# Kernel tuning notes

Measured on AMD Instinct MI355X. Metric: run time of the kernel, lower is better.

## Reference

```python
import jax, jax.numpy as jnp
import numpy as np

# Static discretization grid (torch version computes this on host from data;
# with inputs in [0,1) the clamps min(..,-2)-0.1 / max(..,2)+0.1 make it constant).
PPU = 128          # points_per_unit
MULT = 16          # 2 ** rho.num_halving_layers
XMIN, XMAX = -2.1, 2.1
NUM_GRID = int(np.ceil(PPU * (XMAX - XMIN) / MULT) * MULT)  # 544
SIGMA_CH = 1024
RHO_C = 8          # rho in/out channels


def setup_inputs() -> dict:
    key = jax.random.key(0)
    ks = jax.random.split(key, 8)
    B, N, M = 8, 2048, 2048
    log_ls = float(np.log(2.0 / PPU))  # init_length_scale = 2 / points_per_unit
    return {
        "x": jax.random.uniform(ks[0], (B, N, 1), dtype=jnp.float32),
        "y": jax.random.normal(ks[1], (B, N, 1), dtype=jnp.float32),
        "x_out": jax.random.uniform(ks[2], (B, M, 1), dtype=jnp.float32),
        # encoder ConvDeepSet (in_channels = 2: density + y)
        "enc_sigma": jnp.full((2,), log_ls, dtype=jnp.float32),
        "enc_W": jax.random.normal(ks[3], (2, RHO_C), dtype=jnp.float32) * 0.5,
        "enc_b": jnp.zeros((RHO_C,), dtype=jnp.float32),
        # rho stand-in: point-wise linear 8 -> 8
        "rho_W": jax.random.normal(ks[4], (RHO_C, RHO_C), dtype=jnp.float32) * 0.35,
        "rho_b": jnp.zeros((RHO_C,), dtype=jnp.float32),
        # mean FinalLayer (in_channels = rho.out_channels = 8, out_channels = 1)
        "mean_sigma": jnp.full((RHO_C,), log_ls, dtype=jnp.float32),
        "mean_W": jax.random.normal(ks[5], (RHO_C, 1), dtype=jnp.float32) * 0.35,
        "mean_b": jnp.zeros((1,), dtype=jnp.float32),
        # sigma FinalLayer (out_channels = sigma_channels = 1024)
        "sig_sigma": jnp.full((RHO_C,), log_ls, dtype=jnp.float32),
        "sig_W": jax.random.normal(ks[6], (RHO_C, SIGMA_CH), dtype=jnp.float32) * 0.35,
        "sig_b": jnp.zeros((SIGMA_CH,), dtype=jnp.float32),
        "noise_scale": jnp.zeros((1,), dtype=jnp.float32),
    }


def _rbf_weights(a, t, log_sigma):
    # a: (B, n, 1), t: (B, m, 1) -> (B, n, m, C) per-channel RBF weights
    d = (a - jnp.swapaxes(t, 1, 2)) ** 2            # (B, n, m) squared dists
    scales = jnp.exp(log_sigma)                      # (C,)
    return jnp.exp(-0.5 * d[..., None] / scales ** 2)


def reference(x, y, x_out, enc_sigma, enc_W, enc_b, rho_W, rho_b,
              mean_sigma, mean_W, mean_b, sig_sigma, sig_W, sig_b, noise_scale):
    B = x.shape[0]
    grid = jnp.broadcast_to(
        jnp.linspace(XMIN, XMAX, NUM_GRID, dtype=x.dtype)[None, :, None],
        (B, NUM_GRID, 1))

    # --- encoder ConvDeepSet: density channel + value channel, RBF smoothing onto grid
    wt = _rbf_weights(x, grid, enc_sigma)            # (B, N, G, 2)
    y_aug = jnp.concatenate([jnp.ones_like(x), y], axis=-1)  # (B, N, 2)
    F = jnp.einsum('bnc,bngc->bgc', y_aug, wt)       # (B, G, 2)
    den, conv = F[..., :1], F[..., 1:]
    F = jnp.concatenate([den, conv / (den + 1e-8)], axis=-1)
    h = jax.nn.sigmoid(F @ enc_W + enc_b)            # (B, G, 8)

    # --- rho (stand-in point-wise linear CNN)
    h = h @ rho_W + rho_b                            # (B, G, 8)

    # --- mean FinalLayer: RBF set-conv from grid to x_out, then linear
    wt_m = _rbf_weights(grid, x_out, mean_sigma)     # (B, G, M, 8)
    mean = jnp.einsum('bgc,bgmc->bmc', h, wt_m) @ mean_W + mean_b  # (B, M, 1)

    # --- sigma FinalLayer -> basis embedding, inner-product covariance
    wt_s = _rbf_weights(grid, x_out, sig_sigma)      # (B, G, M, 8)
    basis = jnp.einsum('bgc,bgmc->bmc', h, wt_s) @ sig_W + sig_b   # (B, M, 1024)
    cov = jnp.einsum('bmc,bnc->bmn', basis, basis)   # (B, M, M)
    cov = cov + jnp.exp(noise_scale[0]) * jnp.eye(cov.shape[-1], dtype=cov.dtype)
    return mean, cov
```

## Files before the change

### kernel.cpp

```cpp
#include <hip/hip_runtime.h>
#include <math.h>

#define GRID_N 544
#define BATCH  8
#define NPTS   2048
#define MPTS   2048
#define XMIN_F (-2.1f)
#define STEP_F (4.2f / 543.0f)

typedef float v4f __attribute__((ext_vector_type(4)));

#define PRM_OFF 0
#define H_OFF   128
#define FST_OFF (H_OFF + BATCH*GRID_N*8)
#define P_OFF   (FST_OFF + BATCH*8*MPTS)
#define CM_OFF  (P_OFF + BATCH*MPTS*8)

__global__ __launch_bounds__(256) void k_encode(
    const float* __restrict__ x, const float* __restrict__ y,
    const float* __restrict__ enc_sigma,
    const float* __restrict__ enc_W, const float* __restrict__ enc_b,
    const float* __restrict__ rho_W, const float* __restrict__ rho_b,
    const float* __restrict__ mean_sigma, const float* __restrict__ sig_sigma,
    const float* __restrict__ sig_W, const float* __restrict__ sig_b,
    float* __restrict__ prm, float* __restrict__ h_out) {
  int b = blockIdx.y, g = blockIdx.x, t = threadIdx.x;

  if (g == GRID_N) {
    if (b != 0) return;
    __shared__ float part[256];
    {
      int pair = t >> 2, q = t & 3;
      int i = pair >> 3, j = pair & 7;
      float s = 0.f;
      int k0 = q * 256;
      for (int k = k0; k < k0 + 256; ++k) s += sig_W[i*1024+k] * sig_W[j*1024+k];
      part[t] = s;
      __syncthreads();
      if (q == 0) prm[16 + pair] = part[t] + part[t+1] + part[t+2] + part[t+3];
      __syncthreads();
    }
    {
      int ch = t >> 5, lane = t & 31;
      float s = 0.f;
      for (int k = lane; k < 1024; k += 32) s += sig_W[ch*1024+k] * sig_b[k];
      part[t] = s;
      __syncthreads();
      if (lane == 0) {
        float acc = 0.f;
        for (int k = 0; k < 32; ++k) acc += part[(ch<<5)+k];
        prm[80 + ch] = acc;
      }
      __syncthreads();
    }
    if (t < 32) {
      float v = 0.f;
      for (int k = t; k < 1024; k += 32) v += sig_b[k] * sig_b[k];
      part[t] = v;
    }
    __syncthreads();
    if (t == 0) {
      float v = 0.f;
      for (int k = 0; k < 32; ++k) v += part[k];
      prm[88] = v;
    } else if (t == 1) {
      bool f = true;
      for (int c = 0; c < 8; ++c) {
        prm[c]     = 0.5f * __expf(-2.f * mean_sigma[c]);
        prm[8 + c] = 0.5f * __expf(-2.f * sig_sigma[c]);
        if (mean_sigma[c] != mean_sigma[0] || sig_sigma[c] != sig_sigma[0]) f = false;
      }
      if (mean_sigma[0] != sig_sigma[0]) f = false;
      prm[89] = f ? 1.f : 0.f;
    }
    return;
  }

  float gv = XMIN_F + (float)g * STEP_F;
  float es0 = enc_sigma[0], es1 = enc_sigma[1];
  float a0 = 0.5f * __expf(-2.f * es0);
  float a1 = 0.5f * __expf(-2.f * es1);
  bool uni = (es0 == es1);
  const float4* x4 = (const float4*)(x + (size_t)b * NPTS);
  const float4* y4 = (const float4*)(y + (size_t)b * NPTS);
  float s0 = 0.f, s1 = 0.f;
  #pragma unroll
  for (int i = 0; i < 2; ++i) {
    int n = i * 256 + t;
    float4 xv = x4[n], yv = y4[n];
    float dx, d, w;
    dx = xv.x - gv; d = dx*dx; w = __expf(-d*a0); s0 += w;
    s1 += yv.x * (uni ? w : __expf(-d*a1));
    dx = xv.y - gv; d = dx*dx; w = __expf(-d*a0); s0 += w;
    s1 += yv.y * (uni ? w : __expf(-d*a1));
    dx = xv.z - gv; d = dx*dx; w = __expf(-d*a0); s0 += w;
    s1 += yv.z * (uni ? w : __expf(-d*a1));
    dx = xv.w - gv; d = dx*dx; w = __expf(-d*a0); s0 += w;
    s1 += yv.w * (uni ? w : __expf(-d*a1));
  }
  #pragma unroll
  for (int off = 32; off > 0; off >>= 1) {
    s0 += __shfl_down(s0, off);
    s1 += __shfl_down(s1, off);
  }
  __shared__ float w0s[4], w1s[4];
  int wid = t >> 6;
  if ((t & 63) == 0) { w0s[wid] = s0; w1s[wid] = s1; }
  __syncthreads();
  if (t == 0) {
    float den = w0s[0] + w0s[1] + w0s[2] + w0s[3];
    float conv = w1s[0] + w1s[1] + w1s[2] + w1s[3];
    float F0 = den, F1 = conv / (den + 1e-8f);
    float hh[8];
    #pragma unroll
    for (int jj = 0; jj < 8; ++jj) {
      float z = F0 * enc_W[jj] + F1 * enc_W[8 + jj] + enc_b[jj];
      hh[jj] = 1.f / (1.f + __expf(-z));
    }
    #pragma unroll
    for (int jj = 0; jj < 8; ++jj) {
      float v = rho_b[jj];
      #pragma unroll
      for (int ii = 0; ii < 8; ++ii) v += hh[ii] * rho_W[ii*8 + jj];
      h_out[((size_t)b * GRID_N + g) * 8 + jj] = v;
    }
  }
}

__global__ __launch_bounds__(256) void k_feat(
    const float* __restrict__ x_out, const float* __restrict__ mean_W,
    const float* __restrict__ mean_b, const float* __restrict__ prm,
    const float* __restrict__ h, float* __restrict__ mean_out,
    float* __restrict__ fSt, float* __restrict__ Pv, float* __restrict__ cm) {
  int b = blockIdx.y, t = threadIdx.x;
  int ml = t & 63, slice = t >> 6;
  int m = blockIdx.x * 64 + ml;
  float xo = x_out[(size_t)b * MPTS + m];
  bool fused = prm[89] != 0.f;
  float accm[8] = {0,0,0,0,0,0,0,0};
  float accs[8] = {0,0,0,0,0,0,0,0};
  const float* hb = h + (size_t)b * GRID_N * 8;
  const float4* h4 = (const float4*)hb;
  int gbase = slice * 136;
  if (fused) {
    float a = prm[0];
    for (int gg = 0; gg < 136; ++gg) {
      int g = gbase + gg;
      float gv = XMIN_F + (float)g * STEP_F;
      float dx = gv - xo;
      float w = __expf(-(dx*dx) * a);
      float4 h0 = h4[g*2], h1 = h4[g*2+1];
      accm[0] += h0.x * w; accm[1] += h0.y * w;
      accm[2] += h0.z * w; accm[3] += h0.w * w;
      accm[4] += h1.x * w; accm[5] += h1.y * w;
      accm[6] += h1.z * w; accm[7] += h1.w * w;
    }
  } else {
    float am[8], asg[8];
    #pragma unroll
    for (int c = 0; c < 8; ++c) { am[c] = prm[c]; asg[c] = prm[8 + c]; }
    for (int gg = 0; gg < 136; ++gg) {
      int g = gbase + gg;
      float gv = XMIN_F + (float)g * STEP_F;
      float dx = gv - xo;
      float d = dx * dx;
      #pragma unroll
      for (int c = 0; c < 8; ++c) {
        float hv = hb[g*8 + c];
        accm[c] += hv * __expf(-d * am[c]);
        accs[c] += hv * __expf(-d * asg[c]);
      }
    }
  }
  __shared__ float red[256 * 17];
  #pragma unroll
  for (int c = 0; c < 8; ++c) {
    red[t*17 + c] = accm[c];
    if (!fused) red[t*17 + 8 + c] = accs[c];
  }
  __syncthreads();
  if (t < 64) {
    int mm = blockIdx.x * 64 + t;
    float fm[8], fs[8];
    #pragma unroll
    for (int c = 0; c < 8; ++c) {
      fm[c] = red[t*17+c] + red[(t+64)*17+c] + red[(t+128)*17+c] + red[(t+192)*17+c];
    }
    if (fused) {
      #pragma unroll
      for (int c = 0; c < 8; ++c) fs[c] = fm[c];
    } else {
      #pragma unroll
      for (int c = 0; c < 8; ++c) {
        fs[c] = red[t*17+8+c] + red[(t+64)*17+8+c] + red[(t+128)*17+8+c] + red[(t+192)*17+8+c];
      }
    }
    float mv = mean_b[0];
    #pragma unroll
    for (int c = 0; c < 8; ++c) mv += fm[c] * mean_W[c];
    mean_out[(size_t)b * MPTS + mm] = mv;
    float cmv = prm[88];
    #pragma unroll
    for (int c = 0; c < 8; ++c) cmv += fs[c] * prm[80 + c];
    cm[(size_t)b * MPTS + mm] = cmv;
    size_t base = ((size_t)b * MPTS + mm) * 8;
    #pragma unroll
    for (int c2 = 0; c2 < 8; ++c2) {
      float p = prm[80 + c2];
      #pragma unroll
      for (int c = 0; c < 8; ++c) p += fs[c] * prm[16 + c*8 + c2];
      Pv[base + c2] = p;
    }
    float* fp = fSt + (size_t)b * 8 * MPTS + mm;
    #pragma unroll
    for (int c = 0; c < 8; ++c) fp[c * MPTS] = fs[c];
  }
}

__global__ __launch_bounds__(256) void k_cov(
    const float* __restrict__ fSt, const float* __restrict__ Pv,
    const float* __restrict__ cm, const float* __restrict__ noise_scale,
    float* __restrict__ cov) {
  int b = blockIdx.y, t = threadIdx.x;
  int half = blockIdx.x & 1, rt = blockIdx.x >> 1;
  int col = half * 1024 + 4 * t;
  int row0 = rt * 32;
  float noise = __expf(noise_scale[0]);
  v4f fn[8];
  const float* fb = fSt + (size_t)b * 8 * MPTS;
  #pragma unroll
  for (int c = 0; c < 8; ++c)
    fn[c] = *(const v4f*)(fb + c * MPTS + col);
  const float* Pr = Pv + ((size_t)b * MPTS + row0) * 8;
  const float* Cr = cm + (size_t)b * MPTS + row0;
  #pragma unroll 1
  for (int r8 = 0; r8 < 4; ++r8) {
    v4f o[8];
    #pragma unroll
    for (int i = 0; i < 8; ++i) {
      int mi = r8 * 8 + i;
      float cc = Cr[mi];
      float a0 = cc, a1 = cc, a2 = cc, a3 = cc;
      #pragma unroll
      for (int c = 0; c < 8; ++c) {
        float p = Pr[mi * 8 + c];
        a0 += p * fn[c].x; a1 += p * fn[c].y;
        a2 += p * fn[c].z; a3 += p * fn[c].w;
      }
      int mg = row0 + mi;
      if (mg == col)     a0 += noise;
      if (mg == col + 1) a1 += noise;
      if (mg == col + 2) a2 += noise;
      if (mg == col + 3) a3 += noise;
      o[i].x = a0; o[i].y = a1; o[i].z = a2; o[i].w = a3;
    }
    #pragma unroll
    for (int i = 0; i < 8; ++i) {
      int mi = r8 * 8 + i;
      v4f* dst = (v4f*)(cov + ((size_t)b * MPTS + row0 + mi) * MPTS + col);
      __builtin_nontemporal_store(o[i], dst);
    }
  }
}

extern "C" void kernel_launch(void* const* d_in, const int* in_sizes, int n_in,
                              void* d_out, int out_size, void* d_ws, size_t ws_size,
                              hipStream_t stream) {
  const float* x          = (const float*)d_in[0];
  const float* y          = (const float*)d_in[1];
  const float* x_out      = (const float*)d_in[2];
  const float* enc_sigma  = (const float*)d_in[3];
  const float* enc_W      = (const float*)d_in[4];
  const float* enc_b      = (const float*)d_in[5];
  const float* rho_W      = (const float*)d_in[6];
  const float* rho_b      = (const float*)d_in[7];
  const float* mean_sigma = (const float*)d_in[8];
  const float* mean_W     = (const float*)d_in[9];
  const float* mean_b     = (const float*)d_in[10];
  const float* sig_sigma  = (const float*)d_in[11];
  const float* sig_W      = (const float*)d_in[12];
  const float* sig_b      = (const float*)d_in[13];
  const float* noise_sc   = (const float*)d_in[14];

  float* wsf = (float*)d_ws;
  float* prm  = wsf + PRM_OFF;
  float* hbuf = wsf + H_OFF;
  float* fStb = wsf + FST_OFF;
  float* Pb   = wsf + P_OFF;
  float* cmb  = wsf + CM_OFF;

  float* mean_out = (float*)d_out;
  float* cov_out  = mean_out + (size_t)BATCH * MPTS;

  k_encode<<<dim3(GRID_N + 1, BATCH), 256, 0, stream>>>(
      x, y, enc_sigma, enc_W, enc_b, rho_W, rho_b,
      mean_sigma, sig_sigma, sig_W, sig_b, prm, hbuf);
  k_feat<<<dim3(MPTS/64, BATCH), 256, 0, stream>>>(x_out, mean_W, mean_b, prm,
                                                   hbuf, mean_out, fStb, Pb, cmb);
  k_cov<<<dim3(2 * (MPTS/32), BATCH), 256, 0, stream>>>(fStb, Pb, cmb, noise_sc,
                                                        cov_out);
}
```

Measured before the change: 219.7 us.

## Fuse encode, feature and covariance kernels into one cooperative persistent kernel

Replaces the three separate kernel launches with a single cooperative kernel that loops persistently over the encode, feature and covariance work and separates the stages with grid-wide syncs. The aim is to remove inter-kernel launch gaps and tail effects. In exchange it adds two grid barriers and caps the grid by occupancy (at most 1024 blocks), which could underuse the GPU in the bandwidth-bound covariance write stage. It falls back to the old three-kernel path if the cooperative launch fails.

```diff
diff --git a/kernel.cpp b/kernel.cpp
--- a/kernel.cpp
+++ b/kernel.cpp
@@ -1,5 +1,8 @@
 #include <hip/hip_runtime.h>
+#include <hip/hip_cooperative_groups.h>
 #include <math.h>
+
+namespace cg = cooperative_groups;
 
 #define GRID_N 544
 #define BATCH  8
@@ -15,6 +18,267 @@
 #define FST_OFF (H_OFF + BATCH*GRID_N*8)
 #define P_OFF   (FST_OFF + BATCH*8*MPTS)
 #define CM_OFF  (P_OFF + BATCH*MPTS*8)
+
+__global__ __launch_bounds__(256, 4) void k_fused(
+    const float* __restrict__ x, const float* __restrict__ y,
+    const float* __restrict__ x_out,
+    const float* __restrict__ enc_sigma, const float* __restrict__ enc_W,
+    const float* __restrict__ enc_b, const float* __restrict__ rho_W,
+    const float* __restrict__ rho_b, const float* __restrict__ mean_sigma,
+    const float* __restrict__ mean_W, const float* __restrict__ mean_b,
+    const float* __restrict__ sig_sigma, const float* __restrict__ sig_W,
+    const float* __restrict__ sig_b, const float* __restrict__ noise_scale,
+    float* __restrict__ prm, float* __restrict__ h_out,
+    float* __restrict__ fSt, float* __restrict__ Pv, float* __restrict__ cm,
+    float* __restrict__ mean_out, float* __restrict__ cov) {
+  const int bid = blockIdx.x, t = threadIdx.x, nb = gridDim.x;
+  __shared__ float sbuf[256 * 9];
+  __shared__ float w0s[4], w1s[4];
+
+  for (int u = bid; u < BATCH * GRID_N + 1; u += nb) {
+    if (u == BATCH * GRID_N) {
+      {
+        int pair = t >> 2, q = t & 3;
+        int i = pair >> 3, j = pair & 7;
+        float s = 0.f;
+        int k0 = q * 256;
+        for (int k = k0; k < k0 + 256; ++k) s += sig_W[i*1024+k] * sig_W[j*1024+k];
+        sbuf[t] = s;
+        __syncthreads();
+        if (q == 0) prm[16 + pair] = sbuf[t] + sbuf[t+1] + sbuf[t+2] + sbuf[t+3];
+        __syncthreads();
+      }
+      {
+        int ch = t >> 5, lane = t & 31;
+        float s = 0.f;
+        for (int k = lane; k < 1024; k += 32) s += sig_W[ch*1024+k] * sig_b[k];
+        sbuf[t] = s;
+        __syncthreads();
+        if (lane == 0) {
+          float acc = 0.f;
+          for (int k = 0; k < 32; ++k) acc += sbuf[(ch<<5)+k];
+          prm[80 + ch] = acc;
+        }
+        __syncthreads();
+      }
+      if (t < 32) {
+        float v = 0.f;
+        for (int k = t; k < 1024; k += 32) v += sig_b[k] * sig_b[k];
+        sbuf[t] = v;
+      }
+      __syncthreads();
+      if (t == 0) {
+        float v = 0.f;
+        for (int k = 0; k < 32; ++k) v += sbuf[k];
+        prm[88] = v;
+      } else if (t == 1) {
+        bool f = true;
+        for (int c = 0; c < 8; ++c) {
+          prm[c]     = 0.5f * __expf(-2.f * mean_sigma[c]);
+          prm[8 + c] = 0.5f * __expf(-2.f * sig_sigma[c]);
+          if (mean_sigma[c] != mean_sigma[0] || sig_sigma[c] != sig_sigma[0]) f = false;
+        }
+        if (mean_sigma[0] != sig_sigma[0]) f = false;
+        prm[89] = f ? 1.f : 0.f;
+      }
+    } else {
+      int b = u / GRID_N, g = u - b * GRID_N;
+      float gv = XMIN_F + (float)g * STEP_F;
+      float es0 = enc_sigma[0], es1 = enc_sigma[1];
+      float a0 = 0.5f * __expf(-2.f * es0);
+      float a1 = 0.5f * __expf(-2.f * es1);
+      bool uni = (es0 == es1);
+      const float4* x4 = (const float4*)(x + (size_t)b * NPTS);
+      const float4* y4 = (const float4*)(y + (size_t)b * NPTS);
+      float s0 = 0.f, s1 = 0.f;
+      #pragma unroll
+      for (int i = 0; i < 2; ++i) {
+        int n = i * 256 + t;
+        float4 xv = x4[n], yv = y4[n];
+        float dx, d, w;
+        dx = xv.x - gv; d = dx*dx; w = __expf(-d*a0); s0 += w;
+        s1 += yv.x * (uni ? w : __expf(-d*a1));
+        dx = xv.y - gv; d = dx*dx; w = __expf(-d*a0); s0 += w;
+        s1 += yv.y * (uni ? w : __expf(-d*a1));
+        dx = xv.z - gv; d = dx*dx; w = __expf(-d*a0); s0 += w;
+        s1 += yv.z * (uni ? w : __expf(-d*a1));
+        dx = xv.w - gv; d = dx*dx; w = __expf(-d*a0); s0 += w;
+        s1 += yv.w * (uni ? w : __expf(-d*a1));
+      }
+      #pragma unroll
+      for (int off = 32; off > 0; off >>= 1) {
+        s0 += __shfl_down(s0, off);
+        s1 += __shfl_down(s1, off);
+      }
+      int wid = t >> 6;
+      if ((t & 63) == 0) { w0s[wid] = s0; w1s[wid] = s1; }
+      __syncthreads();
+      if (t == 0) {
+        float den = w0s[0] + w0s[1] + w0s[2] + w0s[3];
+        float conv = w1s[0] + w1s[1] + w1s[2] + w1s[3];
+        float F0 = den, F1 = conv / (den + 1e-8f);
+        float hh[8];
+        #pragma unroll
+        for (int jj = 0; jj < 8; ++jj) {
+          float z = F0 * enc_W[jj] + F1 * enc_W[8 + jj] + enc_b[jj];
+          hh[jj] = 1.f / (1.f + __expf(-z));
+        }
+        #pragma unroll
+        for (int jj = 0; jj < 8; ++jj) {
+          float v = rho_b[jj];
+          #pragma unroll
+          for (int ii = 0; ii < 8; ++ii) v += hh[ii] * rho_W[ii*8 + jj];
+          h_out[((size_t)b * GRID_N + g) * 8 + jj] = v;
+        }
+      }
+    }
+    __syncthreads();
+  }
+  cg::this_grid().sync();
+
+  bool fsc = prm[89] != 0.f;
+  for (int fb = bid; fb < BATCH * (MPTS/16); fb += nb) {
+    int b = fb >> 7, mblk = fb & 127;
+    int ml = t & 15, slice = t >> 4;
+    int m = mblk * 16 + ml;
+    float xo = x_out[(size_t)b * MPTS + m];
+    const float* hb = h_out + (size_t)b * GRID_N * 8;
+    const float4* h4 = (const float4*)hb;
+    int gbase = slice * 34;
+    float accm[8] = {0,0,0,0,0,0,0,0};
+    float accs[8] = {0,0,0,0,0,0,0,0};
+    if (fsc) {
+      float a = prm[0];
+      for (int gg = 0; gg < 34; ++gg) {
+        int g = gbase + gg;
+        float gv = XMIN_F + (float)g * STEP_F;
+        float dx = gv - xo;
+        float w = __expf(-(dx*dx) * a);
+        float4 h0 = h4[g*2], h1 = h4[g*2+1];
+        accm[0] += h0.x * w; accm[1] += h0.y * w;
+        accm[2] += h0.z * w; accm[3] += h0.w * w;
+        accm[4] += h1.x * w; accm[5] += h1.y * w;
+        accm[6] += h1.z * w; accm[7] += h1.w * w;
+      }
+    } else {
+      float am[8], asg[8];
+      #pragma unroll
+      for (int c = 0; c < 8; ++c) { am[c] = prm[c]; asg[c] = prm[8 + c]; }
+      for (int gg = 0; gg < 34; ++gg) {
+        int g = gbase + gg;
+        float gv = XMIN_F + (float)g * STEP_F;
+        float dx = gv - xo;
+        float d = dx * dx;
+        #pragma unroll
+        for (int c = 0; c < 8; ++c) {
+          float hv = hb[g*8 + c];
+          accm[c] += hv * __expf(-d * am[c]);
+          accs[c] += hv * __expf(-d * asg[c]);
+        }
+      }
+    }
+    #pragma unroll
+    for (int c = 0; c < 8; ++c) sbuf[t*9 + c] = accm[c];
+    __syncthreads();
+    float fm[8], fs[8];
+    if (t < 16) {
+      #pragma unroll
+      for (int c = 0; c < 8; ++c) {
+        float s = 0.f;
+        #pragma unroll
+        for (int sl = 0; sl < 16; ++sl) s += sbuf[(sl*16 + t)*9 + c];
+        fm[c] = s;
+      }
+    }
+    if (!fsc) {
+      __syncthreads();
+      #pragma unroll
+      for (int c = 0; c < 8; ++c) sbuf[t*9 + c] = accs[c];
+      __syncthreads();
+      if (t < 16) {
+        #pragma unroll
+        for (int c = 0; c < 8; ++c) {
+          float s = 0.f;
+          #pragma unroll
+          for (int sl = 0; sl < 16; ++sl) s += sbuf[(sl*16 + t)*9 + c];
+          fs[c] = s;
+        }
+      }
+    } else {
+      if (t < 16) {
+        #pragma unroll
+        for (int c = 0; c < 8; ++c) fs[c] = fm[c];
+      }
+    }
+    if (t < 16) {
+      int mm = mblk * 16 + t;
+      float mv = mean_b[0];
+      #pragma unroll
+      for (int c = 0; c < 8; ++c) mv += fm[c] * mean_W[c];
+      mean_out[(size_t)b * MPTS + mm] = mv;
+      float cmv = prm[88];
+      #pragma unroll
+      for (int c = 0; c < 8; ++c) cmv += fs[c] * prm[80 + c];
+      cm[(size_t)b * MPTS + mm] = cmv;
+      size_t base = ((size_t)b * MPTS + mm) * 8;
+      #pragma unroll
+      for (int c2 = 0; c2 < 8; ++c2) {
+        float p = prm[80 + c2];
+        #pragma unroll
+        for (int c = 0; c < 8; ++c) p += fs[c] * prm[16 + c*8 + c2];
+        Pv[base + c2] = p;
+      }
+      float* fp = fSt + (size_t)b * 8 * MPTS + mm;
+      #pragma unroll
+      for (int c = 0; c < 8; ++c) fp[c * MPTS] = fs[c];
+    }
+    __syncthreads();
+  }
+  cg::this_grid().sync();
+
+  float noise = __expf(noise_scale[0]);
+  for (int cb = bid; cb < BATCH * 2 * (MPTS/32); cb += nb) {
+    int b = cb >> 7, r = cb & 127;
+    int half = r & 1, rt = r >> 1;
+    int col = half * 1024 + 4 * t;
+    int row0 = rt * 32;
+    v4f fn[8];
+    const float* fb_ = fSt + (size_t)b * 8 * MPTS;
+    #pragma unroll
+    for (int c = 0; c < 8; ++c)
+      fn[c] = *(const v4f*)(fb_ + c * MPTS + col);
+    const float* Pr = Pv + ((size_t)b * MPTS + row0) * 8;
+    const float* Cr = cm + (size_t)b * MPTS + row0;
+    #pragma unroll 1
+    for (int r8 = 0; r8 < 4; ++r8) {
+      v4f o[8];
+      #pragma unroll
+      for (int i = 0; i < 8; ++i) {
+        int mi = r8 * 8 + i;
+        float cc = Cr[mi];
+        float a0 = cc, a1 = cc, a2 = cc, a3 = cc;
+        #pragma unroll
+        for (int c = 0; c < 8; ++c) {
+          float p = Pr[mi * 8 + c];
+          a0 += p * fn[c].x; a1 += p * fn[c].y;
+          a2 += p * fn[c].z; a3 += p * fn[c].w;
+        }
+        int mg = row0 + mi;
+        if (mg == col)     a0 += noise;
+        if (mg == col + 1) a1 += noise;
+        if (mg == col + 2) a2 += noise;
+        if (mg == col + 3) a3 += noise;
+        o[i].x = a0; o[i].y = a1; o[i].z = a2; o[i].w = a3;
+      }
+      #pragma unroll
+      for (int i = 0; i < 8; ++i) {
+        int mi = r8 * 8 + i;
+        v4f* dst = (v4f*)(cov + ((size_t)b * MPTS + row0 + mi) * MPTS + col);
+        __builtin_nontemporal_store(o[i], dst);
+      }
+    }
+  }
+}
 
 __global__ __launch_bounds__(256) void k_encode(
     const float* __restrict__ x, const float* __restrict__ y,
@@ -25,7 +289,6 @@
     const float* __restrict__ sig_W, const float* __restrict__ sig_b,
     float* __restrict__ prm, float* __restrict__ h_out) {
   int b = blockIdx.y, g = blockIdx.x, t = threadIdx.x;
-
   if (g == GRID_N) {
     if (b != 0) return;
     __shared__ float part[256];
@@ -75,7 +338,6 @@
     }
     return;
   }
-
   float gv = XMIN_F + (float)g * STEP_F;
   float es0 = enc_sigma[0], es1 = enc_sigma[1];
   float a0 = 0.5f * __expf(-2.f * es0);
@@ -292,6 +554,28 @@
   float* mean_out = (float*)d_out;
   float* cov_out  = mean_out + (size_t)BATCH * MPTS;
 
+  static int s_grid = 0;
+  if (s_grid == 0) {
+    int bpc = 0;
+    hipError_t qe = hipOccupancyMaxActiveBlocksPerMultiprocessor(&bpc, k_fused, 256, 0);
+    int g = (qe == hipSuccess && bpc > 0) ? bpc * 256 : 0;
+    if (g > 1024) g = 1024;
+    s_grid = (g >= 64) ? g : -1;
+  }
+
+  if (s_grid > 0) {
+    void* args[] = {(void*)&x, (void*)&y, (void*)&x_out, (void*)&enc_sigma,
+                    (void*)&enc_W, (void*)&enc_b, (void*)&rho_W, (void*)&rho_b,
+                    (void*)&mean_sigma, (void*)&mean_W, (void*)&mean_b,
+                    (void*)&sig_sigma, (void*)&sig_W, (void*)&sig_b,
+                    (void*)&noise_sc, (void*)&prm, (void*)&hbuf, (void*)&fStb,
+                    (void*)&Pb, (void*)&cmb, (void*)&mean_out, (void*)&cov_out};
+    hipError_t e = hipLaunchCooperativeKernel((void*)k_fused, dim3(s_grid),
+                                              dim3(256), args, 0, stream);
+    if (e == hipSuccess) return;
+    s_grid = -1;
+  }
+
   k_encode<<<dim3(GRID_N + 1, BATCH), 256, 0, stream>>>(
       x, y, enc_sigma, enc_W, enc_b, rho_W, rho_b,
       mean_sigma, sig_sigma, sig_W, sig_b, prm, hbuf);
```

Result: slower. 352.1 us (+60.2%).
